# Performance work log

Measured on AMD Instinct MI355X. Metric: run time of the kernel, lower is better.

Reference implementation:

```python
import jax, jax.numpy as jnp
import numpy as np
from jax import lax

P = 0.1  # WTA keep fraction (mode='per_image')


def setup_inputs() -> dict:
    key = jax.random.key(0)
    x = jax.random.normal(key, (32, 256, 64, 64), dtype=jnp.float32)
    return {"x": x}


def reference(x) -> jnp.ndarray:
    bs, nc, sz, _ = x.shape
    k = int(np.ceil(nc * sz * sz * P))  # 104858 for these shapes
    flat = x.reshape(bs, -1)                      # [bs, nc*sz*sz]
    topk_vals = lax.top_k(flat, k)[0]             # [bs, k], descending
    thr = topk_vals[:, -1].reshape(bs, 1, 1, 1)   # k-th largest per image
    return x * (x >= thr).astype(x.dtype)
```

## Files before the change

### kernel.cpp

```cpp
#include <hip/hip_runtime.h>
#include <hip/hip_bf16.h>
#include <stdint.h>


#define IMGS    32
#define NPER    1048576
#define NPER4   (NPER / 4)
#define NBINS   8192
#define BPI     64
#define MARGIN  8192u
#define CAPC    98304
#define LCAP    2048
#define CSTRIDE 64

typedef float floatx4 __attribute__((ext_vector_type(4)));

__device__ __forceinline__ unsigned mapf(float f) {
    unsigned u = __float_as_uint(f);
    return (u & 0x80000000u) ? ~u : (u | 0x80000000u);
}

__device__ __forceinline__ void block_scan256(unsigned* p, int t, unsigned v) {
    p[t] = v;
    __syncthreads();
    #pragma unroll
    for (int off = 1; off < 256; off <<= 1) {
        unsigned u = (t >= off) ? p[t - off] : 0u;
        __syncthreads();
        p[t] += u;
        __syncthreads();
    }
}

__global__ void k_sample(const float4* __restrict__ x4, uint2* __restrict__ win,
                         unsigned* __restrict__ cnt_hi, unsigned* __restrict__ candCnt,
                         unsigned k) {
    __shared__ unsigned h[NBINS];
    __shared__ unsigned pre[256];
    __shared__ unsigned s_hi, s_lo;
    int t = threadIdx.x, img = blockIdx.x;
    if (t == 0) { cnt_hi[img * CSTRIDE] = 0u; candCnt[img * CSTRIDE] = 0u; }
    for (int j = t; j < NBINS; j += 256) h[j] = 0u;
    __syncthreads();

    long long ib = (long long)img * NPER4;
    for (int c = 0; c < 64; ++c) {
        float4 v = x4[ib + (long long)c * 4096 + t];
        atomicAdd(&h[mapf(v.x) >> 19], 1u);
        atomicAdd(&h[mapf(v.y) >> 19], 1u);
        atomicAdd(&h[mapf(v.z) >> 19], 1u);
        atomicAdd(&h[mapf(v.w) >> 19], 1u);
    }
    __syncthreads();

    unsigned s = 0;
    #pragma unroll
    for (int j = 0; j < 32; ++j) s += h[t * 32 + ((j + t) & 31)];
    block_scan256(pre, t, s);
    unsigned above = pre[255] - pre[t];

    unsigned tk_hi = (k > MARGIN) ? (k - MARGIN) : 1u;
    unsigned tk_lo = k + MARGIN;
    unsigned tgt_hi = (tk_hi + 15u) >> 4;
    unsigned tgt_lo = (tk_lo + 15u) >> 4;

    if (above < tgt_hi && above + s >= tgt_hi) {
        unsigned cum = above;
        for (int j = 31; j >= 0; --j) {
            unsigned v = h[t * 32 + j];
            cum += v;
            if (cum >= tgt_hi) { s_hi = (unsigned)(t * 32 + j); break; }
        }
    }
    if (above < tgt_lo && above + s >= tgt_lo) {
        unsigned cum = above;
        for (int j = 31; j >= 0; --j) {
            unsigned v = h[t * 32 + j];
            cum += v;
            if (cum >= tgt_lo) { s_lo = (unsigned)(t * 32 + j); break; }
        }
    }
    __syncthreads();
    if (t == 0) {
        unsigned shi = s_hi, slo = s_lo;
        if (shi - slo > 15u) slo = shi - 15u;
        unsigned hi_key = (shi >= 8191u) ? 0xFFFFFFFFu : ((shi + 1u) << 19);
        unsigned lo_key = slo << 19;
        win[img] = make_uint2(lo_key, hi_key);
    }
}

__global__ void k_count(const float4* __restrict__ x4, const uint2* __restrict__ win,
                        unsigned* __restrict__ cnt_hi, unsigned* __restrict__ candCnt,
                        unsigned* __restrict__ candKey) {
    __shared__ unsigned lkey[LCAP];
    __shared__ unsigned red[256];
    __shared__ unsigned lcnt, gbase;
    int t = threadIdx.x, bx = blockIdx.x, img = bx >> 6;
    if (t == 0) lcnt = 0u;
    __syncthreads();

    uint2 w = win[img];
    unsigned c = 0;
    long long base4 = (long long)img * NPER4 + (long long)(bx & 63) * 4096;
    for (int it = 0; it < 16; ++it) {
        float4 v = x4[base4 + it * 256 + t];
        float* vp = &v.x;
        #pragma unroll
        for (int j = 0; j < 4; ++j) {
            unsigned key = mapf(vp[j]);
            c += (key >= w.y) ? 1u : 0u;
            if (key >= w.x && key < w.y) {
                unsigned p = atomicAdd(&lcnt, 1u);
                if (p < LCAP) lkey[p] = key;
            }
        }
    }
    red[t] = c;
    __syncthreads();
    for (int off = 128; off > 0; off >>= 1) {
        if (t < off) red[t] += red[t + off];
        __syncthreads();
    }
    unsigned n = lcnt;
    if (n > LCAP) n = LCAP;
    if (t == 0) {
        atomicAdd(&cnt_hi[img * CSTRIDE], red[0]);
        gbase = atomicAdd(&candCnt[img * CSTRIDE], n);
    }
    __syncthreads();
    unsigned gb = gbase;
    long long cb = (long long)img * CAPC;
    for (unsigned j = t; j < n; j += 256u) {
        unsigned pos = gb + j;
        if (pos < CAPC) candKey[cb + pos] = lkey[j];
    }
}

__global__ void k_select(const uint2* __restrict__ win,
                         const unsigned* __restrict__ cnt_hi,
                         const unsigned* __restrict__ candCnt,
                         const unsigned* __restrict__ candKey,
                         unsigned* __restrict__ thrArr, unsigned k) {
    int img = blockIdx.x, t = threadIdx.x;
    __shared__ unsigned h2[2048];
    __shared__ unsigned pre[256];
    __shared__ unsigned sbin, srank;

    unsigned n = candCnt[img * CSTRIDE];
    if (n > CAPC) n = CAPC;
    unsigned chi = cnt_hi[img * CSTRIDE];
    unsigned r = (k > chi) ? (k - chi) : 1u;
    if (r > n) r = n;
    unsigned lo = win[img].x;
    const uint4* ck4 = (const uint4*)(candKey + (long long)img * CAPC);
    unsigned n4 = (n + 3u) >> 2;

    const int shifts[3] = {12, 4, 0};
    const int fshift[3] = {31, 12, 4};
    const int binsA[3]  = {2048, 256, 16};
    unsigned pfx = 0u;
    for (int rd = 0; rd < 3; ++rd) {
        int bins = binsA[rd];
        for (int j = t; j < bins; j += 256) h2[j] = 0u;
        __syncthreads();
        int sh = shifts[rd], fs = fshift[rd];
        unsigned bmask = (unsigned)bins - 1u;
        bool nofilt = (rd == 0);
        #pragma unroll 2
        for (unsigned j = t; j < n4; j += 256u) {
            uint4 kk = ck4[j];
            unsigned base = j * 4u;
            unsigned kw[4] = {kk.x, kk.y, kk.z, kk.w};
            #pragma unroll
            for (int c = 0; c < 4; ++c) {
                if (base + (unsigned)c < n) {
                    unsigned delta = kw[c] - lo;
                    bool ok = nofilt || ((delta >> fs) == pfx);
                    if (ok) atomicAdd(&h2[(delta >> sh) & bmask], 1u);
                }
            }
        }
        __syncthreads();

        int bpt = bins >> 8; if (bpt < 1) bpt = 1;
        unsigned s = 0;
        if (t * bpt < bins)
            for (int j = 0; j < bpt; ++j) s += h2[t * bpt + j];
        block_scan256(pre, t, s);
        unsigned above = pre[255] - pre[t];
        if (above < r && above + s >= r) {
            unsigned cum = above;
            for (int j = bpt - 1; j >= 0; --j) {
                unsigned v = h2[t * bpt + j];
                cum += v;
                if (cum >= r) {
                    sbin = (unsigned)(t * bpt + j);
                    srank = r - (cum - v);
                    break;
                }
            }
        }
        __syncthreads();
        pfx = (pfx << (rd == 0 ? 11 : (rd == 1 ? 8 : 4))) | sbin;
        r = srank;
        __syncthreads();
    }
    if (t == 0) thrArr[img] = lo + pfx;
}

__global__ void k_mask(const float4* __restrict__ x4, float4* __restrict__ o4,
                       const unsigned* __restrict__ thrArr) {
    int bx = blockIdx.x, t = threadIdx.x, img = bx >> 6;
    unsigned thr = thrArr[img];
    long long base4 = (long long)img * NPER4 + (long long)(bx & 63) * 4096;
    for (int it = 0; it < 16; ++it) {
        long long i = base4 + it * 256 + t;
        float4 v = x4[i];
        float4 o;
        o.x = (mapf(v.x) >= thr) ? v.x : 0.0f;
        o.y = (mapf(v.y) >= thr) ? v.y : 0.0f;
        o.z = (mapf(v.z) >= thr) ? v.z : 0.0f;
        o.w = (mapf(v.w) >= thr) ? v.w : 0.0f;
        floatx4 ov = { o.x, o.y, o.z, o.w };
        __builtin_nontemporal_store(ov, (floatx4*)&o4[i]);
    }
}

extern "C" void kernel_launch(void* const* d_in, const int* in_sizes, int n_in,
                              void* d_out, int out_size, void* d_ws, size_t ws_size,
                              hipStream_t stream) {
    const float* x = (const float*)d_in[0];
    float* out = (float*)d_out;
    unsigned k = (unsigned)((NPER + 9) / 10);

    char* ws = (char*)d_ws;
    size_t padB = (size_t)IMGS * CSTRIDE * 4;
    unsigned* cnt_hi  = (unsigned*)ws;
    unsigned* candCnt = (unsigned*)(ws + padB);
    uint2*    win     = (uint2*)   (ws + 2 * padB);
    unsigned* thrArr  = (unsigned*)(ws + 2 * padB + 1024);
    unsigned* candKey = (unsigned*)(ws + 2 * padB + 2048);

    dim3 blk(256);
    k_sample<<<dim3(IMGS), blk, 0, stream>>>((const float4*)x, win, cnt_hi, candCnt, k);
    k_count<<<dim3(IMGS * BPI), blk, 0, stream>>>((const float4*)x, win,
                                                  cnt_hi, candCnt, candKey);
    k_select<<<dim3(IMGS), blk, 0, stream>>>(win, cnt_hi, candCnt, candKey, thrArr, k);
    k_mask<<<dim3(IMGS * BPI), blk, 0, stream>>>((const float4*)x, (float4*)out, thrArr);
}
```

Baseline: 129.6 us.

## Fuse mask write into count pass and fix up window candidates by index

```diff
diff --git a/kernel.cpp b/kernel.cpp
--- a/kernel.cpp
+++ b/kernel.cpp
@@ -44,12 +44,19 @@
     __syncthreads();
 
     long long ib = (long long)img * NPER4;
-    for (int c = 0; c < 64; ++c) {
-        float4 v = x4[ib + (long long)c * 4096 + t];
-        atomicAdd(&h[mapf(v.x) >> 19], 1u);
-        atomicAdd(&h[mapf(v.y) >> 19], 1u);
-        atomicAdd(&h[mapf(v.z) >> 19], 1u);
-        atomicAdd(&h[mapf(v.w) >> 19], 1u);
+    for (int c = 0; c < 16; ++c) {
+        float4 a = x4[ib + (long long)(c      ) * 4096 + t];
+        float4 b = x4[ib + (long long)(c + 16) * 4096 + t];
+        float4 d = x4[ib + (long long)(c + 32) * 4096 + t];
+        float4 e = x4[ib + (long long)(c + 48) * 4096 + t];
+        atomicAdd(&h[mapf(a.x) >> 19], 1u); atomicAdd(&h[mapf(a.y) >> 19], 1u);
+        atomicAdd(&h[mapf(a.z) >> 19], 1u); atomicAdd(&h[mapf(a.w) >> 19], 1u);
+        atomicAdd(&h[mapf(b.x) >> 19], 1u); atomicAdd(&h[mapf(b.y) >> 19], 1u);
+        atomicAdd(&h[mapf(b.z) >> 19], 1u); atomicAdd(&h[mapf(b.w) >> 19], 1u);
+        atomicAdd(&h[mapf(d.x) >> 19], 1u); atomicAdd(&h[mapf(d.y) >> 19], 1u);
+        atomicAdd(&h[mapf(d.z) >> 19], 1u); atomicAdd(&h[mapf(d.w) >> 19], 1u);
+        atomicAdd(&h[mapf(e.x) >> 19], 1u); atomicAdd(&h[mapf(e.y) >> 19], 1u);
+        atomicAdd(&h[mapf(e.z) >> 19], 1u); atomicAdd(&h[mapf(e.w) >> 19], 1u);
     }
     __syncthreads();
 
@@ -90,10 +97,12 @@
     }
 }
 
-__global__ void k_count(const float4* __restrict__ x4, const uint2* __restrict__ win,
-                        unsigned* __restrict__ cnt_hi, unsigned* __restrict__ candCnt,
-                        unsigned* __restrict__ candKey) {
+__global__ void k_count_mask(const float4* __restrict__ x4, float4* __restrict__ o4,
+                             const uint2* __restrict__ win,
+                             unsigned* __restrict__ cnt_hi, unsigned* __restrict__ candCnt,
+                             unsigned* __restrict__ candKey, unsigned* __restrict__ candIdx) {
     __shared__ unsigned lkey[LCAP];
+    __shared__ unsigned lidx[LCAP];
     __shared__ unsigned red[256];
     __shared__ unsigned lcnt, gbase;
     int t = threadIdx.x, bx = blockIdx.x, img = bx >> 6;
@@ -104,17 +113,25 @@
     unsigned c = 0;
     long long base4 = (long long)img * NPER4 + (long long)(bx & 63) * 4096;
     for (int it = 0; it < 16; ++it) {
-        float4 v = x4[base4 + it * 256 + t];
+        long long i = base4 + it * 256 + t;
+        float4 v = x4[i];
+        unsigned ebase = (unsigned)(i & (NPER4 - 1)) * 4u;
+        float4 o;
         float* vp = &v.x;
+        float* op = &o.x;
         #pragma unroll
         for (int j = 0; j < 4; ++j) {
-            unsigned key = mapf(vp[j]);
+            float cv = vp[j];
+            unsigned key = mapf(cv);
             c += (key >= w.y) ? 1u : 0u;
+            op[j] = (key >= w.x) ? cv : 0.0f;
             if (key >= w.x && key < w.y) {
                 unsigned p = atomicAdd(&lcnt, 1u);
-                if (p < LCAP) lkey[p] = key;
+                if (p < LCAP) { lkey[p] = key; lidx[p] = ebase + (unsigned)j; }
             }
         }
+        floatx4 ov = { o.x, o.y, o.z, o.w };
+        __builtin_nontemporal_store(ov, (floatx4*)&o4[i]);
     }
     red[t] = c;
     __syncthreads();
@@ -133,7 +150,10 @@
     long long cb = (long long)img * CAPC;
     for (unsigned j = t; j < n; j += 256u) {
         unsigned pos = gb + j;
-        if (pos < CAPC) candKey[cb + pos] = lkey[j];
+        if (pos < CAPC) {
+            candKey[cb + pos] = lkey[j];
+            candIdx[cb + pos] = lidx[j];
+        }
     }
 }
 
@@ -143,7 +163,7 @@
                          const unsigned* __restrict__ candKey,
                          unsigned* __restrict__ thrArr, unsigned k) {
     int img = blockIdx.x, t = threadIdx.x;
-    __shared__ unsigned h2[2048];
+    __shared__ unsigned h2[4096];
     __shared__ unsigned pre[256];
     __shared__ unsigned sbin, srank;
 
@@ -156,37 +176,31 @@
     const uint4* ck4 = (const uint4*)(candKey + (long long)img * CAPC);
     unsigned n4 = (n + 3u) >> 2;
 
-    const int shifts[3] = {12, 4, 0};
-    const int fshift[3] = {31, 12, 4};
-    const int binsA[3]  = {2048, 256, 16};
     unsigned pfx = 0u;
-    for (int rd = 0; rd < 3; ++rd) {
-        int bins = binsA[rd];
+    for (int rd = 0; rd < 2; ++rd) {
+        int bins = rd == 0 ? 2048 : 4096;
+        int sh = rd == 0 ? 12 : 0;
         for (int j = t; j < bins; j += 256) h2[j] = 0u;
         __syncthreads();
-        int sh = shifts[rd], fs = fshift[rd];
         unsigned bmask = (unsigned)bins - 1u;
-        bool nofilt = (rd == 0);
-        #pragma unroll 2
         for (unsigned j = t; j < n4; j += 256u) {
             uint4 kk = ck4[j];
             unsigned base = j * 4u;
             unsigned kw[4] = {kk.x, kk.y, kk.z, kk.w};
             #pragma unroll
-            for (int c = 0; c < 4; ++c) {
-                if (base + (unsigned)c < n) {
-                    unsigned delta = kw[c] - lo;
-                    bool ok = nofilt || ((delta >> fs) == pfx);
+            for (int c2 = 0; c2 < 4; ++c2) {
+                if (base + (unsigned)c2 < n) {
+                    unsigned delta = kw[c2] - lo;
+                    bool ok = (rd == 0) || ((delta >> 12) == pfx);
                     if (ok) atomicAdd(&h2[(delta >> sh) & bmask], 1u);
                 }
             }
         }
         __syncthreads();
 
-        int bpt = bins >> 8; if (bpt < 1) bpt = 1;
+        int bpt = bins >> 8;
         unsigned s = 0;
-        if (t * bpt < bins)
-            for (int j = 0; j < bpt; ++j) s += h2[t * bpt + j];
+        for (int j = 0; j < bpt; ++j) s += h2[t * bpt + ((j + t) & (bpt - 1))];
         block_scan256(pre, t, s);
         unsigned above = pre[255] - pre[t];
         if (above < r && above + s >= r) {
@@ -202,28 +216,26 @@
             }
         }
         __syncthreads();
-        pfx = (pfx << (rd == 0 ? 11 : (rd == 1 ? 8 : 4))) | sbin;
+        pfx = (rd == 0) ? sbin : ((pfx << 12) | sbin);
         r = srank;
         __syncthreads();
     }
     if (t == 0) thrArr[img] = lo + pfx;
 }
 
-__global__ void k_mask(const float4* __restrict__ x4, float4* __restrict__ o4,
-                       const unsigned* __restrict__ thrArr) {
+__global__ void k_fixup(float* __restrict__ out, const unsigned* __restrict__ thrArr,
+                        const unsigned* __restrict__ candCnt,
+                        const unsigned* __restrict__ candKey,
+                        const unsigned* __restrict__ candIdx) {
     int bx = blockIdx.x, t = threadIdx.x, img = bx >> 6;
+    unsigned n = candCnt[img * CSTRIDE];
+    if (n > CAPC) n = CAPC;
     unsigned thr = thrArr[img];
-    long long base4 = (long long)img * NPER4 + (long long)(bx & 63) * 4096;
-    for (int it = 0; it < 16; ++it) {
-        long long i = base4 + it * 256 + t;
-        float4 v = x4[i];
-        float4 o;
-        o.x = (mapf(v.x) >= thr) ? v.x : 0.0f;
-        o.y = (mapf(v.y) >= thr) ? v.y : 0.0f;
-        o.z = (mapf(v.z) >= thr) ? v.z : 0.0f;
-        o.w = (mapf(v.w) >= thr) ? v.w : 0.0f;
-        floatx4 ov = { o.x, o.y, o.z, o.w };
-        __builtin_nontemporal_store(ov, (floatx4*)&o4[i]);
+    const unsigned* ck = candKey + (long long)img * CAPC;
+    const unsigned* ci = candIdx + (long long)img * CAPC;
+    float* oi = out + (long long)img * NPER;
+    for (unsigned j = (unsigned)(bx & 63) * 256u + t; j < n; j += 64u * 256u) {
+        if (ck[j] < thr) oi[ci[j]] = 0.0f;
     }
 }
 
@@ -241,11 +253,14 @@
     uint2*    win     = (uint2*)   (ws + 2 * padB);
     unsigned* thrArr  = (unsigned*)(ws + 2 * padB + 1024);
     unsigned* candKey = (unsigned*)(ws + 2 * padB + 2048);
+    unsigned* candIdx = (unsigned*)(ws + 2 * padB + 2048
+                                       + (size_t)IMGS * CAPC * 4);
 
     dim3 blk(256);
     k_sample<<<dim3(IMGS), blk, 0, stream>>>((const float4*)x, win, cnt_hi, candCnt, k);
-    k_count<<<dim3(IMGS * BPI), blk, 0, stream>>>((const float4*)x, win,
-                                                  cnt_hi, candCnt, candKey);
+    k_count_mask<<<dim3(IMGS * BPI), blk, 0, stream>>>((const float4*)x, (float4*)out,
+                                                       win, cnt_hi, candCnt,
+                                                       candKey, candIdx);
     k_select<<<dim3(IMGS), blk, 0, stream>>>(win, cnt_hi, candCnt, candKey, thrArr, k);
-    k_mask<<<dim3(IMGS * BPI), blk, 0, stream>>>((const float4*)x, (float4*)out, thrArr);
-}
+    k_fixup<<<dim3(IMGS * BPI), blk, 0, stream>>>(out, thrArr, candCnt, candKey, candIdx);
+}
```

Result: faster. 118.5 us (-8.6%).
